# Optimization experiments

Hardware: AMD Instinct MI355X
Metric: run time of the kernel (lower is better)

Reference implementation:

```python
import jax, jax.numpy as jnp
import numpy as np

B, S, D = 4, 4096, 1024


def setup_inputs() -> dict:
    key = jax.random.key(0)
    ks = jax.random.split(key, 4)
    scale = 1.0 / np.sqrt(D)
    x = jax.random.normal(ks[0], (B, S, D), dtype=jnp.float32)
    Wg = jax.random.normal(ks[1], (D, D), dtype=jnp.float32) * scale
    Wv = jax.random.normal(ks[2], (D, D), dtype=jnp.float32) * scale
    Wd = jax.random.normal(ks[3], (D, D), dtype=jnp.float32) * scale
    bg = jnp.zeros((D,), dtype=jnp.float32)
    bv = jnp.zeros((D,), dtype=jnp.float32)
    bd = jnp.ones((D,), dtype=jnp.float32)  # decay_bias_init = 1.0
    return {"x": x, "Wg": Wg, "bg": bg, "Wv": Wv, "bv": bv, "Wd": Wd, "bd": bd}


def _scan_causal(x_scan, a):
    # h_t = a_t * h_{t-1} + x_t, scanned over time; x_scan, a: [B,S,D]
    def step(h, inp):
        a_t, x_t = inp
        h = a_t * h + x_t
        return h, h

    h0 = jnp.zeros(x_scan.shape[::2], dtype=x_scan.dtype)  # [B,D]
    xs = (jnp.swapaxes(a, 0, 1), jnp.swapaxes(x_scan, 0, 1))  # [S,B,D]
    _, out = jax.lax.scan(step, h0, xs)
    return jnp.swapaxes(out, 0, 1)  # back to [B,S,D]


def reference(x, Wg, bg, Wv, bv, Wd, bd):
    # nn.Linear: y = x @ W.T + b
    g = jnp.einsum('bsd,ed->bse', x, Wg) + bg
    v = jnp.einsum('bsd,ed->bse', x, Wv) + bv
    d = jnp.einsum('bsd,ed->bse', x, Wd) + bd
    x_scan = jax.nn.sigmoid(g) * jnp.tanh(v)
    a = 0.001 + 0.998 * jax.nn.sigmoid(d)
    return _scan_causal(x_scan, a)
```

## Files before the change

### kernel.cpp

```cpp
#include <hip/hip_runtime.h>
#include <cstddef>
#include <cstdint>


typedef _Float16 f16;
typedef f16 f16x8 __attribute__((ext_vector_type(8)));
typedef float f32x4 __attribute__((ext_vector_type(4)));

#define S_LEN 4096
#define D_DIM 1024
#define B_DIM 4
#define M_TOT (B_DIM * S_LEN)
#define N_TOT (3 * D_DIM)
#define K_TOT D_DIM

#define CLEN 16
#define CPB (S_LEN / CLEN)
#define NCHUNK (B_DIM * CPB)

#define SEG 16
#define NSEG (CPB / SEG)

__device__ __forceinline__ void cvt8(const float* s, f16* d) {
  f32x4 a = *(const f32x4*)s;
  f32x4 b = *(const f32x4*)(s + 4);
  f16x8 o;
  o[0] = (f16)a[0]; o[1] = (f16)a[1]; o[2] = (f16)a[2]; o[3] = (f16)a[3];
  o[4] = (f16)b[0]; o[5] = (f16)b[1]; o[6] = (f16)b[2]; o[7] = (f16)b[3];
  *(f16x8*)d = o;
}

__global__ void cvt_all_kernel(const float* __restrict__ x, const float* __restrict__ w0,
                               const float* __restrict__ w1, const float* __restrict__ w2,
                               f16* __restrict__ Ah, f16* __restrict__ Bh) {
  int i = (blockIdx.x * 256 + threadIdx.x) * 8;
  if (i < M_TOT * K_TOT) {
    cvt8(x + i, Ah + i);
  } else {
    int w = i - M_TOT * K_TOT;
    int row = w >> 10;
    int col = w & 1023;
    int srow = row / 3;
    int mat = row - srow * 3;
    const float* s = (mat == 0) ? w0 : (mat == 1) ? w1 : w2;
    cvt8(s + srow * 1024 + col, Bh + w);
  }
}

#define BM 256
#define BN 192
#define BK 64
#define RAWP 200
#define XSP 72

#define AS_OFF 0
#define BS_OFF 32768
#define ABUF 16384
#define BBUF 12288
#define SMEM_H 57344

__device__ __forceinline__ void gl_lds16(const void* g, void* l) {
  __builtin_amdgcn_global_load_lds((const __attribute__((address_space(1))) void*)g,
                                   (__attribute__((address_space(3))) void*)l, 16, 0, 0);
}

__device__ __forceinline__ void act(float g, float v, float d, f16& xh, f16& ah) {
  float sg = 1.f / (1.f + __expf(-g));
  float tv = 1.f - 2.f / (__expf(2.f * v) + 1.f);
  float sd = 1.f / (1.f + __expf(-d));
  xh = (f16)(sg * tv);
  ah = (f16)(0.001f + 0.998f * sd);
}

__global__ __launch_bounds__(512, 2) void gemm_fused_kernel(
    const f16* __restrict__ A, const f16* __restrict__ Bt,
    const float* __restrict__ bg, const float* __restrict__ bv,
    const float* __restrict__ bd,
    f16* __restrict__ xsA, f16* __restrict__ aA,
    float* __restrict__ P, float* __restrict__ H) {
  __shared__ __attribute__((aligned(16))) f16 smem[SMEM_H];
  const int tid = threadIdx.x;
  const int lane = tid & 63;
  const int wave = tid >> 6;

  const int wg = blockIdx.x;
  const int orig = (wg & 7) * 128 + (wg >> 3);
  const int bx = orig & 15;
  const int by = orig >> 4;
  const int m0 = by * BM;
  const int bn0 = bx * BN;

  const int srow = tid >> 3;
  const int sslot = (tid & 7) ^ (srow & 7);
  const f16* aSrc = A + (size_t)(m0 + srow) * K_TOT + sslot * 8;
  const f16* bSrc = Bt + (size_t)(bn0 + srow) * K_TOT + sslot * 8;
  f16* aDst0 = smem + AS_OFF + tid * 8;
  f16* bDst0 = smem + BS_OFF + tid * 8;

  const int wm = (wave >> 1) * 64;
  const int wn = (wave & 1) * 96;
  const int lm = lane & 15;
  const int q = lane >> 4;
  const int sw0 = ((0 * 4 + q) ^ (lm & 7)) * 8;
  const int sw1 = ((1 * 4 + q) ^ (lm & 7)) * 8;

  f32x4 acc[4][6] = {};

#pragma unroll
  for (int r = 0; r < 4; ++r)
    gl_lds16(aSrc + (size_t)r * 64 * K_TOT, aDst0 + r * 4096);
#pragma unroll
  for (int r = 0; r < 3; ++r)
    gl_lds16(bSrc + (size_t)r * 64 * K_TOT, bDst0 + r * 4096);
  __syncthreads();

  for (int t = 0; t < 16; ++t) {
    const int cur = t & 1;
    if (t < 15) {
      const int nxt = cur ^ 1;
      const size_t k0 = (size_t)(t + 1) * BK;
#pragma unroll
      for (int r = 0; r < 4; ++r)
        gl_lds16(aSrc + (size_t)r * 64 * K_TOT + k0, aDst0 + nxt * ABUF + r * 4096);
#pragma unroll
      for (int r = 0; r < 3; ++r)
        gl_lds16(bSrc + (size_t)r * 64 * K_TOT + k0, bDst0 + nxt * BBUF + r * 4096);
    }
    const f16* Acur = smem + AS_OFF + cur * ABUF;
    const f16* Bcur = smem + BS_OFF + cur * BBUF;
#pragma unroll
    for (int kk = 0; kk < 2; ++kk) {
      const int sw = kk ? sw1 : sw0;
      f16x8 af[4], bf[6];
#pragma unroll
      for (int i = 0; i < 4; ++i)
        af[i] = *(const f16x8*)&Acur[(wm + i * 16 + lm) * BK + sw];
#pragma unroll
      for (int j = 0; j < 6; ++j)
        bf[j] = *(const f16x8*)&Bcur[(wn + j * 16 + lm) * BK + sw];
#pragma unroll
      for (int i = 0; i < 4; ++i)
#pragma unroll
        for (int j = 0; j < 6; ++j)
          acc[i][j] = __builtin_amdgcn_mfma_f32_16x16x32_f16(af[i], bf[j], acc[i][j], 0, 0, 0);
    }
    __syncthreads();
  }

  f16* Raw = smem;
  f16* xsL = smem + 25600;
  f16* aLs = smem + 34816;
  const int d = tid & 63;
  const int cc = tid >> 6;
  const int gd = (bx << 6) + d;
  const float Bg = bg[gd], Bv = bv[gd], Bd_ = bd[gd];

#pragma unroll
  for (int half = 0; half < 2; ++half) {
    if ((wave >> 2) == half) {
      const int r0 = ((wave >> 1) & 1) * 64 + ((lane >> 4) << 2);
      const int c0 = wn + (lane & 15);
#pragma unroll
      for (int i = 0; i < 4; ++i)
#pragma unroll
        for (int j = 0; j < 6; ++j)
#pragma unroll
          for (int r = 0; r < 4; ++r)
            Raw[(r0 + i * 16 + r) * RAWP + c0 + j * 16] = (f16)acc[i][j][r];
    }
    __syncthreads();

    {
      float p = 1.f, h = 0.f;
#pragma unroll
      for (int i = 0; i < CLEN; ++i) {
        const int r = cc * CLEN + i;
        const f16* t3 = &Raw[r * RAWP + 3 * d];
        f16 xh, ah;
        act((float)t3[0] + Bg, (float)t3[1] + Bv, (float)t3[2] + Bd_, xh, ah);
        xsL[r * XSP + d] = xh;
        aLs[r * XSP + d] = ah;
        float xf = (float)xh, af_ = (float)ah;
        h = af_ * h + xf;
        p *= af_;
      }
      const int gs = (m0 >> 4) + half * 8 + cc;
      P[(size_t)gs * D_DIM + gd] = p;
      H[(size_t)gs * D_DIM + gd] = h;
    }
    __syncthreads();

#pragma unroll
    for (int rr = 0; rr < 2; ++rr) {
      const int row = rr * 64 + (tid >> 3);
      const int col = (tid & 7) * 8;
      const size_t gi = (size_t)(m0 + half * 128 + row) * D_DIM + (bx << 6) + col;
      *(f16x8*)(xsA + gi) = *(const f16x8*)&xsL[row * XSP + col];
      *(f16x8*)(aA + gi) = *(const f16x8*)&aLs[row * XSP + col];
    }
    __syncthreads();
  }
}

__global__ void scan2a_kernel(const float* __restrict__ P, const float* __restrict__ H,
                              float* __restrict__ SP, float* __restrict__ SH) {
  const int u = blockIdx.x * 256 + threadIdx.x;
  const int d = u & 1023;
  const int s = (u >> 10) & (NSEG - 1);
  const int b = u >> 14;
  const int gs0 = b * CPB + s * SEG;
  float p = 1.f, h = 0.f;
#pragma unroll 4
  for (int c = 0; c < SEG; ++c) {
    const size_t off = (size_t)(gs0 + c) * D_DIM + d;
    const float pp = P[off], hh = H[off];
    h = pp * h + hh;
    p *= pp;
  }
  const size_t so = (size_t)(b * NSEG + s) * D_DIM + d;
  SP[so] = p;
  SH[so] = h;
}

__global__ void scan2bc_kernel(const float* __restrict__ P, const float* __restrict__ H,
                               const float* __restrict__ SP, const float* __restrict__ SH,
                               float* __restrict__ carry) {
  const int u = blockIdx.x * 256 + threadIdx.x;
  const int d = u & 1023;
  const int s = (u >> 10) & (NSEG - 1);
  const int b = u >> 14;
  float h = 0.f;
  for (int s2 = 0; s2 < s; ++s2) {
    const size_t off = (size_t)(b * NSEG + s2) * D_DIM + d;
    h = SP[off] * h + SH[off];
  }
  const int gs0 = b * CPB + s * SEG;
#pragma unroll 4
  for (int c = 0; c < SEG; ++c) {
    const size_t off = (size_t)(gs0 + c) * D_DIM + d;
    carry[off] = h;
    h = P[off] * h + H[off];
  }
}

__global__ void scan3_kernel(const f16* __restrict__ xsA, const f16* __restrict__ aA,
                             const float* __restrict__ carry, float* __restrict__ out) {
  const int u = blockIdx.x * 256 + threadIdx.x;
  const int cg = u & 127;
  const int b = (u >> 7) & 3;
  const int ck = u >> 9;
  const int ch = cg * 8;
  const int base = (b * CPB + ck) * D_DIM + ch;
  float h[8];
  *(f32x4*)h = *(const f32x4*)(carry + base);
  *(f32x4*)(h + 4) = *(const f32x4*)(carry + base + 4);
  const int t0 = ck * CLEN;
#pragma unroll 2
  for (int t = t0; t < t0 + CLEN; ++t) {
    const size_t m = (size_t)b * S_LEN + t;
    f16x8 xs8 = *(const f16x8*)(xsA + m * D_DIM + ch);
    f16x8 a8 = *(const f16x8*)(aA + m * D_DIM + ch);
#pragma unroll
    for (int j = 0; j < 8; ++j) h[j] = (float)a8[j] * h[j] + (float)xs8[j];
    float* op = out + m * D_DIM + ch;
    *(f32x4*)op = *(f32x4*)h;
    *(f32x4*)(op + 4) = *(f32x4*)(h + 4);
  }
}

extern "C" void kernel_launch(void* const* d_in, const int* in_sizes, int n_in,
                              void* d_out, int out_size, void* d_ws, size_t ws_size,
                              hipStream_t stream) {
  const float* x = (const float*)d_in[0];
  const float* Wg = (const float*)d_in[1];
  const float* bg = (const float*)d_in[2];
  const float* Wv = (const float*)d_in[3];
  const float* bv = (const float*)d_in[4];
  const float* Wd = (const float*)d_in[5];
  const float* bd = (const float*)d_in[6];
  float* out = (float*)d_out;

  char* ws = (char*)d_ws;
  f16* Ah = (f16*)(ws);
  f16* Bh = (f16*)(ws + 33554432);
  f16* xsA = (f16*)(ws + 39845888);
  f16* aA = (f16*)(ws + 73400320);
  float* P = (float*)(ws + 106954752);
  float* H = (float*)(ws + 111149056);
  float* carry = (float*)(ws + 115343360);
  float* SP = (float*)(ws);
  float* SH = (float*)(ws + 262144);

  cvt_all_kernel<<<9728, 256, 0, stream>>>(x, Wg, Wv, Wd, Ah, Bh);
  gemm_fused_kernel<<<1024, 512, 0, stream>>>(Ah, Bh, bg, bv, bd, xsA, aA, P, H);
  scan2a_kernel<<<256, 256, 0, stream>>>(P, H, SP, SH);
  scan2bc_kernel<<<256, 256, 0, stream>>>(P, H, SP, SH, carry);
  scan3_kernel<<<512, 256, 0, stream>>>(xsA, aA, carry, out);
}
```

Measured before the change: 285.7 us.

## Prefetch two K-tiles ahead with vmcnt waits and fold segment scan into GEMM

The GEMM main loop now issues loads two tiles ahead and waits with explicit vmcnt counts and raw s_barrier instead of a full __syncthreads per iteration, with raised wave priority around the MFMA block. The per-block chunk summaries are also combined in LDS into segment summaries, which removes the separate scan2a launch and its re-read of P/H. SP/SH move to their own workspace region, and the scan3 unroll goes from 2 to 4. The hand-counted vmcnt depends on the exact number of outstanding loads per stage, so getting it wrong would break correctness.

```diff
diff --git a/kernel.cpp b/kernel.cpp
--- a/kernel.cpp
+++ b/kernel.cpp
@@ -77,7 +77,8 @@
     const float* __restrict__ bg, const float* __restrict__ bv,
     const float* __restrict__ bd,
     f16* __restrict__ xsA, f16* __restrict__ aA,
-    float* __restrict__ P, float* __restrict__ H) {
+    float* __restrict__ P, float* __restrict__ H,
+    float* __restrict__ SP, float* __restrict__ SH) {
   __shared__ __attribute__((aligned(16))) f16 smem[SMEM_H];
   const int tid = threadIdx.x;
   const int lane = tid & 63;
@@ -90,6 +91,11 @@
   const int m0 = by * BM;
   const int bn0 = bx * BN;
 
+  const int d = tid & 63;
+  const int cc = tid >> 6;
+  const int gd = (bx << 6) + d;
+  const float Bg = bg[gd], Bv = bv[gd], Bd_ = bd[gd];
+
   const int srow = tid >> 3;
   const int sslot = (tid & 7) ^ (srow & 7);
   const f16* aSrc = A + (size_t)(m0 + srow) * K_TOT + sslot * 8;
@@ -106,28 +112,31 @@
 
   f32x4 acc[4][6] = {};
 
-#pragma unroll
-  for (int r = 0; r < 4; ++r)
-    gl_lds16(aSrc + (size_t)r * 64 * K_TOT, aDst0 + r * 4096);
-#pragma unroll
-  for (int r = 0; r < 3; ++r)
-    gl_lds16(bSrc + (size_t)r * 64 * K_TOT, bDst0 + r * 4096);
-  __syncthreads();
+  auto STAGE = [&](int tile, int buf) {
+    const size_t k0 = (size_t)tile * BK;
+#pragma unroll
+    for (int r = 0; r < 4; ++r)
+      gl_lds16(aSrc + (size_t)r * 64 * K_TOT + k0, aDst0 + buf * ABUF + r * 4096);
+#pragma unroll
+    for (int r = 0; r < 3; ++r)
+      gl_lds16(bSrc + (size_t)r * 64 * K_TOT + k0, bDst0 + buf * BBUF + r * 4096);
+  };
+
+  STAGE(0, 0);
+  STAGE(1, 1);
 
   for (int t = 0; t < 16; ++t) {
-    const int cur = t & 1;
     if (t < 15) {
-      const int nxt = cur ^ 1;
-      const size_t k0 = (size_t)(t + 1) * BK;
-#pragma unroll
-      for (int r = 0; r < 4; ++r)
-        gl_lds16(aSrc + (size_t)r * 64 * K_TOT + k0, aDst0 + nxt * ABUF + r * 4096);
-#pragma unroll
-      for (int r = 0; r < 3; ++r)
-        gl_lds16(bSrc + (size_t)r * 64 * K_TOT + k0, bDst0 + nxt * BBUF + r * 4096);
-    }
-    const f16* Acur = smem + AS_OFF + cur * ABUF;
-    const f16* Bcur = smem + BS_OFF + cur * BBUF;
+      asm volatile("s_waitcnt vmcnt(7)" ::: "memory");
+    } else {
+      asm volatile("s_waitcnt vmcnt(0)" ::: "memory");
+    }
+    __builtin_amdgcn_s_barrier();
+    __builtin_amdgcn_sched_barrier(0);
+
+    const f16* Acur = smem + AS_OFF + (t & 1) * ABUF;
+    const f16* Bcur = smem + BS_OFF + (t & 1) * BBUF;
+    __builtin_amdgcn_s_setprio(1);
 #pragma unroll
     for (int kk = 0; kk < 2; ++kk) {
       const int sw = kk ? sw1 : sw0;
@@ -144,16 +153,21 @@
         for (int j = 0; j < 6; ++j)
           acc[i][j] = __builtin_amdgcn_mfma_f32_16x16x32_f16(af[i], bf[j], acc[i][j], 0, 0, 0);
     }
-    __syncthreads();
-  }
+    __builtin_amdgcn_s_setprio(0);
+    __builtin_amdgcn_sched_barrier(0);
+
+    if (t < 14) {
+      __builtin_amdgcn_s_barrier();
+      STAGE(t + 2, t & 1);
+    }
+  }
+  __syncthreads();
 
   f16* Raw = smem;
   f16* xsL = smem + 25600;
   f16* aLs = smem + 34816;
-  const int d = tid & 63;
-  const int cc = tid >> 6;
-  const int gd = (bx << 6) + d;
-  const float Bg = bg[gd], Bv = bv[gd], Bd_ = bd[gd];
+  float* segP = (float*)(smem + 44032);
+  float* segH = segP + 1024;
 
 #pragma unroll
   for (int half = 0; half < 2; ++half) {
@@ -187,6 +201,8 @@
       const int gs = (m0 >> 4) + half * 8 + cc;
       P[(size_t)gs * D_DIM + gd] = p;
       H[(size_t)gs * D_DIM + gd] = h;
+      segP[(half * 8 + cc) * 64 + d] = p;
+      segH[(half * 8 + cc) * 64 + d] = h;
     }
     __syncthreads();
 
@@ -200,26 +216,20 @@
     }
     __syncthreads();
   }
-}
-
-__global__ void scan2a_kernel(const float* __restrict__ P, const float* __restrict__ H,
-                              float* __restrict__ SP, float* __restrict__ SH) {
-  const int u = blockIdx.x * 256 + threadIdx.x;
-  const int d = u & 1023;
-  const int s = (u >> 10) & (NSEG - 1);
-  const int b = u >> 14;
-  const int gs0 = b * CPB + s * SEG;
-  float p = 1.f, h = 0.f;
-#pragma unroll 4
-  for (int c = 0; c < SEG; ++c) {
-    const size_t off = (size_t)(gs0 + c) * D_DIM + d;
-    const float pp = P[off], hh = H[off];
-    h = pp * h + hh;
-    p *= pp;
-  }
-  const size_t so = (size_t)(b * NSEG + s) * D_DIM + d;
-  SP[so] = p;
-  SH[so] = h;
+
+  if (tid < 64) {
+    float ps = 1.f, hs = 0.f;
+#pragma unroll
+    for (int s = 0; s < 16; ++s) {
+      const float pp = segP[s * 64 + tid];
+      const float hh = segH[s * 64 + tid];
+      hs = pp * hs + hh;
+      ps *= pp;
+    }
+    const size_t so = (size_t)by * D_DIM + (bx << 6) + tid;
+    SP[so] = ps;
+    SH[so] = hs;
+  }
 }
 
 __global__ void scan2bc_kernel(const float* __restrict__ P, const float* __restrict__ H,
@@ -255,7 +265,7 @@
   *(f32x4*)h = *(const f32x4*)(carry + base);
   *(f32x4*)(h + 4) = *(const f32x4*)(carry + base + 4);
   const int t0 = ck * CLEN;
-#pragma unroll 2
+#pragma unroll 4
   for (int t = t0; t < t0 + CLEN; ++t) {
     const size_t m = (size_t)b * S_LEN + t;
     f16x8 xs8 = *(const f16x8*)(xsA + m * D_DIM + ch);
@@ -288,12 +298,11 @@
   float* P = (float*)(ws + 106954752);
   float* H = (float*)(ws + 111149056);
   float* carry = (float*)(ws + 115343360);
-  float* SP = (float*)(ws);
-  float* SH = (float*)(ws + 262144);
+  float* SP = (float*)(ws + 119537664);
+  float* SH = (float*)(ws + 119799808);
 
   cvt_all_kernel<<<9728, 256, 0, stream>>>(x, Wg, Wv, Wd, Ah, Bh);
-  gemm_fused_kernel<<<1024, 512, 0, stream>>>(Ah, Bh, bg, bv, bd, xsA, aA, P, H);
-  scan2a_kernel<<<256, 256, 0, stream>>>(P, H, SP, SH);
+  gemm_fused_kernel<<<1024, 512, 0, stream>>>(Ah, Bh, bg, bv, bd, xsA, aA, P, H, SP, SH);
   scan2bc_kernel<<<256, 256, 0, stream>>>(P, H, SP, SH, carry);
   scan3_kernel<<<512, 256, 0, stream>>>(xsA, aA, carry, out);
 }
```

After: 295.6 us (median of 2 runs). 3.5% more time.
